# Performance work log

Measured on AMD Instinct MI355X. Metric: run time of the kernel, lower is better.

## Reference

```python
import jax, jax.numpy as jnp
import numpy as np

B = 256; SEED = 120; PRED = 24; D = 126; H = 1024
J = 14; JD = 9; HEADS = 4; DH = H // HEADS; SPLH = 128
PARENTS = (-1, -1, 0, 1, 2, 3, -1, 6, -1, -1, 8, 9, 10, 11)  # sparse SPL kinematic tree


def setup_inputs() -> dict:
    key = jax.random.key(0)
    ks = jax.random.split(key, 18)
    s = 0.02
    w = lambda k, shape: jax.random.normal(k, shape, dtype=jnp.float32) * s
    return {
        "poses": jax.random.normal(ks[0], (B, SEED + PRED, D), dtype=jnp.float32),
        "gru_Wih": w(ks[1], (3 * H, D)), "gru_Whh": w(ks[2], (3 * H, H)),
        "gru_bih": w(ks[3], (3 * H,)), "gru_bhh": w(ks[4], (3 * H,)),
        "pre_W": w(ks[5], (H, H)), "pre_b": w(ks[6], (H,)),
        "fp_W": w(ks[7], (H, D)), "fp_b": w(ks[8], (H,)),
        "inproj_W": w(ks[9], (3 * H, H)), "inproj_b": w(ks[10], (3 * H,)),
        "outproj_W": w(ks[11], (H, H)), "outproj_b": w(ks[12], (H,)),
        # per-joint SPL MLPs, stacked; root joints see zero-padded parent slot
        "spl_W1": w(ks[13], (J, SPLH, H + JD)), "spl_b1": w(ks[14], (J, SPLH)),
        "spl_W2": w(ks[15], (J, JD, SPLH)), "spl_b2": w(ks[16], (J, JD)),
    }


def _gru_cell(x, h, Wih, Whh, bih, bhh):
    gi = x @ Wih.T + bih
    gh = h @ Whh.T + bhh
    ir, iz, inn = jnp.split(gi, 3, axis=-1)
    hr, hz, hn = jnp.split(gh, 3, axis=-1)
    r = jax.nn.sigmoid(ir + hr)
    z = jax.nn.sigmoid(iz + hz)
    n = jnp.tanh(inn + r * hn)
    return (1.0 - z) * n + z * h


def _forward(poses, gru_Wih, gru_Whh, gru_bih, gru_bhh, pre_W, pre_b,
             fp_W, fp_b, inproj_W, inproj_b, outproj_W, outproj_b,
             spl_W1, spl_b1, spl_W2, spl_b2):
    input_seq = poses[:, :SEED]  # (B, T_in, D)
    # --- DCT motion attention (rFFT proxy) ---
    freq = jnp.fft.rfft(input_seq, axis=1).real          # (B, F, D), F = SEED//2+1
    feat = freq @ fp_W.T + fp_b                          # (B, F, H)
    qkv = feat @ inproj_W.T + inproj_b
    q, k, v = jnp.split(qkv, 3, axis=-1)
    hsplit = lambda t: t.reshape(t.shape[0], t.shape[1], HEADS, DH)
    q, k, v = hsplit(q), hsplit(k), hsplit(v)
    att = jax.nn.softmax(jnp.einsum('bqhd,bkhd->bhqk', q, k) / np.sqrt(DH).astype(np.float32), axis=-1)
    ctx = jnp.einsum('bhqk,bkhd->bqhd', att, v).reshape(feat.shape)
    attn_out = ctx @ outproj_W.T + outproj_b
    motion_ctx = attn_out.mean(axis=1)                   # (B, H)
    # --- GRU encode over seed ---
    h0 = jnp.zeros((poses.shape[0], H), dtype=poses.dtype)
    def enc(h, x):
        return _gru_cell(x, h, gru_Wih, gru_Whh, gru_bih, gru_bhh), None
    h, _ = jax.lax.scan(enc, h0, jnp.swapaxes(input_seq, 0, 1))
    x_last = input_seq[:, -1]
    # --- hierarchical SPL (sparse mode) ---
    def spl(hid):
        zero = jnp.zeros((hid.shape[0], JD), dtype=hid.dtype)
        preds = [None] * J
        for j in range(J):
            p = PARENTS[j]
            par = zero if p == -1 else preds[p]
            inp = jnp.concatenate([hid, par], axis=-1)   # (B, H+JD)
            hh = jax.nn.relu(inp @ spl_W1[j].T + spl_b1[j])
            preds[j] = jnp.tanh(hh @ spl_W2[j].T + spl_b2[j])
        return jnp.concatenate(preds, axis=-1)            # (B, J*JD)
    def dec(carry, _):
        x, hc = carry
        hc = _gru_cell(x, hc, gru_Wih, gru_Whh, gru_bih, gru_bhh)
        hid = jax.nn.relu(hc @ pre_W.T + pre_b) + motion_ctx
        x = x + spl(hid)
        return (x, hc), x
    _, ys = jax.lax.scan(dec, (x_last, h), None, length=PRED)
    return jnp.swapaxes(ys, 0, 1)                         # (B, PRED, D)


def reference(poses, gru_Wih, gru_Whh, gru_bih, gru_bhh, pre_W, pre_b,
              fp_W, fp_b, inproj_W, inproj_b, outproj_W, outproj_b,
              spl_W1, spl_b1, spl_W2, spl_b2):
    return _forward(poses, gru_Wih, gru_Whh, gru_bih, gru_bhh, pre_W, pre_b,
                    fp_W, fp_b, inproj_W, inproj_b, outproj_W, outproj_b,
                    spl_W1, spl_b1, spl_W2, spl_b2)
```

## Files before the change

kernel.cpp:

```cpp
#include <hip/hip_runtime.h>
#include <hip/hip_bf16.h>

typedef __hip_bfloat16 bf16;
typedef __attribute__((ext_vector_type(8))) short v8bf;
typedef __attribute__((ext_vector_type(16))) float f32x16;
typedef __attribute__((ext_vector_type(4))) float f32x4;
typedef unsigned long long ull;

#define B_    256
#define SEED_ 120
#define PRED_ 24
#define D_    126
#define H_    1024
#define F_    61
#define HEADS_ 4
#define DH_   256

#define GLD16(lds, g) __builtin_amdgcn_global_load_lds( \
    (const __attribute__((address_space(1))) unsigned int*)(g), \
    (__attribute__((address_space(3))) unsigned int*)(lds), 16, 0, 0)
#define VMWAIT(n) asm volatile("s_waitcnt vmcnt(" #n ")" ::: "memory")
#define BARRIER() do { __builtin_amdgcn_s_barrier(); __builtin_amdgcn_sched_barrier(0); } while(0)
#define AL(P) __hip_atomic_load((P), __ATOMIC_RELAXED, __HIP_MEMORY_SCOPE_AGENT)

// ... 45 lines not shown
  float v = (c < D_) ? poses[((size_t)b*(SEED_+PRED_) + (SEED_-1))*D_ + c] : 0.f;
  if (c < D_) x[b*D_ + c] = v;
  xpk[((b>>5)*4 + (c>>5))*1024 + (b&31)*32 + (c&31)] = __float2bfloat16(v);
}

__global__ void c_bf(const float* __restrict__ s, bf16* __restrict__ d, int n){
  int i = blockIdx.x*256 + threadIdx.x;
  if (i < n) d[i] = __float2bfloat16(s[i]);
}

__global__ void c_fpwt(const float* __restrict__ fpW, bf16* __restrict__ o){
  int dd = blockIdx.x;
  for (int k = threadIdx.x; k < H_; k += 256)
    o[(size_t)dd*H_ + k] = __float2bfloat16(dd < D_ ? fpW[(size_t)k*D_ + dd] : 0.f);
}

__global__ void c_wcat(const float* __restrict__ Wih, const float* __restrict__ Whh, bf16* __restrict__ o){
  int r = blockIdx.x;
  int jr; bool hasx, hash;
  if (r < 2048){ jr = r; hasx = true; hash = true; }
  else if (r < 3072){ jr = r; hasx = true; hash = false; }
  else { jr = r - 1024; hasx = false; hash = true; }
  bf16* row = o + (size_t)r*1152;
  for (int c = threadIdx.x; c < 1152; c += 256){
    float v = 0.f;
    if (c < D_) { if (hasx) v = Wih[(size_t)jr*D_ + c]; }
    else if (c >= 128){ if (hash) v = Whh[(size_t)jr*H_ + (c-128)]; }
    row[c] = __float2bfloat16(v);
  }
}

__global__ void c_bcat(const float* __restrict__ bih, const float* __restrict__ bhh, float* __restrict__ o){
  int r = blockIdx.x*256 + threadIdx.x;
  if (r >= 4096) return;
  float v;
  if (r < 2048) v = bih[r] + bhh[r];
  else if (r < 3072) v = bih[r];
  else v = bhh[r - 1024];
  o[r] = v;
}

__global__ __launch_bounds__(256) void c_wpk(const bf16* __restrict__ Wcat, bf16* __restrict__ Wpk){
  int chunk = blockIdx.x*4 + (threadIdx.x >> 6);
  int l = threadIdx.x & 63;
  int ks = chunk % 36; int t2 = chunk / 36; int g = t2 % 3; int ub = t2 / 3;
  int unit = ub*16 + (l & 15);
  bf16* dst = Wpk + (size_t)chunk*512 + l*8;
  #pragma unroll
  for (int e = 0; e < 8; ++e){
    int k = ks*32 + (l>>4)*8 + e;
    int row = (g==0) ? unit : (g==1) ? (1024+unit) : (k < 128 ? 2048+unit : 3072+unit);
    dst[e] = Wcat[(size_t)row*1152 + k];
  }
}

__global__ __launch_bounds__(256) void c_w1pk(const float* __restrict__ sW1, bf16* __restrict__ w1pk){
  int chunk = blockIdx.x*4 + (threadIdx.x >> 6);
  int l = threadIdx.x & 63;
  int ks = chunk & 31, ng = chunk >> 5;
  int unit = ng*16 + (l & 15);
  int j = unit >> 7, rr = unit & 127;
  bf16* dst = w1pk + (size_t)chunk*512 + l*8;
  #pragma unroll
  for (int e = 0; e < 8; ++e){
    int k = ks*32 + (l>>4)*8 + e;
    dst[e] = __float2bfloat16(sW1[((size_t)j*128 + rr)*1033 + k]);
  }
}

__global__ void c_w1par(const float* __restrict__ sW1, float* __restrict__ w1par){
  int i = blockIdx.x*256 + threadIdx.x;
  if (i < 14*9*128){
    int j = i / (9*128); int rem = i % (9*128); int ii = rem / 128; int th = rem % 128;
    w1par[i] = sW1[((size_t)(j*128 + th))*1033 + 1024 + ii];
  }
}

__global__ __launch_bounds__(256) void k_bc(const float* __restrict__ inW, const float* __restrict__ inb,
                     const float* __restrict__ fpb, float* __restrict__ bc){
  int wave = threadIdx.x >> 6, lane = threadIdx.x & 63;
  int r = blockIdx.x*4 + wave;
  const float4* row = (const float4*)(inW + (size_t)r*H_);
  const float4* fp4 = (const float4*)fpb;
  float s = 0.f;
  #pragma unroll
  for (int i = 0; i < 4; ++i){
    float4 a = row[lane + i*64];
    float4 b = fp4[lane + i*64];
    s += a.x*b.x + a.y*b.y + a.z*b.z + a.w*b.w;
  }
  #pragma unroll
  for (int off = 32; off; off >>= 1) s += __shfl_down(s, off);
  if (lane == 0) bc[r] = s + inb[r];
}

#define SLCP(QA, QB, KS, GACC) { \
  union { ull u[2]; v8bf v; } cc_; cc_.u[0]=(QA); cc_.u[1]=(QB); \
  v8bf a_ = cc_.v; \
  v8bf w0_ = *(const v8bf*)&Wl[(0*36+(KS))*512 + lane*8]; \
  v8bf w1_ = *(const v8bf*)&Wl[(1*36+(KS))*512 + lane*8]; \
  v8bf w2_ = *(const v8bf*)&Wl[(2*36+(KS))*512 + lane*8]; \
  aR = __builtin_amdgcn_mfma_f32_16x16x32_bf16(a_, w0_, aR, 0,0,0); \
  aZ = __builtin_amdgcn_mfma_f32_16x16x32_bf16(a_, w1_, aZ, 0,0,0); \
  GACC = __builtin_amdgcn_mfma_f32_16x16x32_bf16(a_, w2_, GACC, 0,0,0); }

#define LDHA(DA, DB, C) { \
// ... 96 lines not shown
    SLCP(a1,b1,25,aN) LDXP(a1,b1,t+1,1)
    SLCP(a2,b2,26,aN) LDXP(a2,b2,t+1,2)
    SLCP(a3,b3,27,aN) LDXP(a3,b3,t+1,3)
    SLCP(a4,b4,28,aN)
    SLCP(a5,b5,29,aN)
    SLCP(a6,b6,30,aN)
    SLCP(a7,b7,31,aN)
    SLCP(a8,b8,32,aN)
    SLCP(a9,b9,33,aN)
    SLCP(a10,b10,34,aN)
    SLCP(a11,b11,35,aN)

    bf16* hd = (t & 1) ? hpk0 : hpk1;
    const bool last = (t == nsteps-1);
    #pragma unroll
    for (int r = 0; r < 4; ++r){
      float rg = 1.f/(1.f + __expf(-(aR[r] + bR)));
      float zg = 1.f/(1.f + __expf(-(aZ[r] + bZ)));
      float ng = tanhf((aI[r] + bI) + rg*(aN[r] + bN));
      float hv = (1.f - zg)*ng + zg*hr[r];
      hr[r] = hv;
      bf16 hv16 = __float2bfloat16(hv);
      unsigned short hbits = *(unsigned short*)&hv16;
      __hip_atomic_store((unsigned short*)(hd + pwb + (size_t)(lb*4 + r)*32), hbits,
                         __ATOMIC_RELAXED, __HIP_MEMORY_SCOPE_AGENT);
      if (last){
        hout_plain[(size_t)(r0 + lb*4 + r)*1024 + ucol] = hv;
        if (hbplain) hbplain[(size_t)(r0 + lb*4 + r)*1024 + ucol] = __float2bfloat16(hv);
      }
    }
    if (coop && t + 1 < nsteps){
      VMWAIT(0);
      __syncthreads();
      if (tid == 0)
        __hip_atomic_store(&prog[q*64 + ub], (unsigned)(t+1), __ATOMIC_RELAXED, __HIP_MEMORY_SCOPE_AGENT);
    }
  }
}

__constant__ int LVJ[14] = {0,1,6,8,9, 2,3,7,10,11, 4,5,12,13};
__constant__ int LVO[4]  = {0,5,10,14};
__constant__ int PAR_[14] = {-1,-1,0,1,2,3,-1,6,-1,-1,8,9,10,11};

#define DGRL(S,C) { const ull* p_=(const ull*)(hspk + hbase + (size_t)(C)*1024); qa##S=AL(p_); qb##S=AL(p_+1); }
#define DGXL(S,C) { const ull* p_=(const ull*)(xpk + xbase + (size_t)(C)*1024); qa##S=AL(p_); qb##S=AL(p_+1); }
#define DGRC(S,KS,GACC) { union{ull u[2];v8bf v;}c_; c_.u[0]=qa##S;c_.u[1]=qb##S; v8bf a_=c_.v; \
  v8bf w0_=*(const v8bf*)&Wl[(KS)*512+lane*8]; \
  v8bf w1_=*(const v8bf*)&Wl[18432+(KS)*512+lane*8]; \
  v8bf w2_=*(const v8bf*)&Wl[36864+(KS)*512+lane*8]; \
  aR=__builtin_amdgcn_mfma_f32_16x16x32_bf16(a_,w0_,aR,0,0,0); \
  aZ=__builtin_amdgcn_mfma_f32_16x16x32_bf16(a_,w1_,aZ,0,0,0); \
  GACC=__builtin_amdgcn_mfma_f32_16x16x32_bf16(a_,w2_,GACC,0,0,0); }

__global__ __launch_bounds__(256) void gru_spl(
    const bf16* __restrict__ xpk, const bf16* __restrict__ Wpk,
    const float* __restrict__ bcat,
    const float* __restrict__ hin_plain, float* __restrict__ hout_plain,
    bf16* __restrict__ hbplain,
    const bf16* __restrict__ hspk, bf16* __restrict__ hdpk,
    const float* __restrict__ hhpre, const float* __restrict__ w1par,
    const float* __restrict__ sW2, const float* __restrict__ sb2,
    float* __restrict__ xcur, bf16* __restrict__ xpkw, float* __restrict__ out,
    int dt, unsigned* __restrict__ progS)
{
  __shared__ bf16 Wl[3*36*512];
  __shared__ float hhl[1792];
  __shared__ float preds_s[128];
  __shared__ float hh_s[128];
  const int tid = threadIdx.x, wave = tid >> 6, lane = tid & 63;
  const int bid = blockIdx.x;
  const int ub = bid & 63, q = bid >> 6, u0 = ub*16;

  {
    const bf16* wsrc = Wpk + (size_t)ub*(3*36*512);
    #pragma unroll
    for (int i = 0; i < 27; ++i){ int c = i*256 + tid; GLD16(&Wl[c*8], wsrc + (size_t)c*8); }
  }

  const int brow = bid, th = tid;
  if (dt > 0){
    for (int i = tid; i < 1792; i += 256) hhl[i] = hhpre[(size_t)brow*1792 + i];
    __syncthreads();
    for (int L = 0; L < 3; ++L){
      for (int ji = LVO[L]; ji < LVO[L+1]; ++ji){
        int j = LVJ[ji], p = PAR_[j];
        if (tid < 128){
          float a0s = hhl[j*128 + th];
          if (p >= 0){
            #pragma unroll
            for (int ii = 0; ii < 9; ++ii)
              a0s += w1par[(j*9 + ii)*128 + th] * preds_s[p*9 + ii];
          }
          hh_s[th] = fmaxf(a0s, 0.f);
        }
        __syncthreads();
        if (tid < 18){
          int oi = th >> 1, half = th & 1;
          const float4* w4 = (const float4*)(sW2 + (size_t)(j*9 + oi)*128 + half*64);
          float s = 0.f;
          #pragma unroll
          for (int q2 = 0; q2 < 16; ++q2){
            float4 wv = w4[q2];
            s += hh_s[half*64 + q2*4 + 0]*wv.x + hh_s[half*64 + q2*4 + 1]*wv.y
               + hh_s[half*64 + q2*4 + 2]*wv.z + hh_s[half*64 + q2*4 + 3]*wv.w;
          }
          s += __shfl_xor(s, 1);
          if (half == 0) preds_s[j*9 + oi] = tanhf(s + sb2[j*9 + oi]);
        }
        __syncthreads();
      }
    }
    if (tid < D_){
      int d = tid;
      size_t xi = (size_t)brow*D_ + d;
      float v = xcur[xi] + preds_s[d];
      xcur[xi] = v;
      bf16 v16 = __float2bfloat16(v);
      __hip_atomic_store((unsigned short*)(xpkw + ((size_t)(brow>>5)*4 + (d>>5))*1024 + (brow&31)*32 + (d&31)),
                         *(unsigned short*)&v16, __ATOMIC_RELAXED, __HIP_MEMORY_SCOPE_AGENT);
      out[((size_t)brow*PRED_ + (dt-1))*D_ + d] = v;
    }
    VMWAIT(0);
    __syncthreads();
    if (tid == 0)
      __hip_atomic_store(&progS[bid], (unsigned)dt, __ATOMIC_RELAXED, __HIP_MEMORY_SCOPE_AGENT);
  }

  VMWAIT(0); BARRIER();

  const int la = lane & 15, lb = lane >> 4;
  const int r0 = q*64 + wave*16;
  const int rb = r0 >> 5, y = wave & 1;
  const int ucol = u0 + la;
  const float bR = bcat[ucol], bZ = bcat[1024+ucol], bI = bcat[2048+ucol], bN = bcat[3072+ucol];
  const size_t hbase = (size_t)rb*32768 + (size_t)y*512 + la*32 + lb*8;
  const size_t xbase = (size_t)rb*4096  + (size_t)y*512 + la*32 + lb*8;
  const size_t pwb = (size_t)rb*32768 + (size_t)(u0>>5)*1024 + (size_t)y*512 + (u0&16) + la;

  float hr[4];
  #pragma unroll
  for (int r = 0; r < 4; ++r) hr[r] = hin_plain[(size_t)(r0 + lb*4 + r)*1024 + ucol];

  ull qa0,qa1,qa2,qa3,qa4,qa5,qa6,qa7,qa8,qa9,qa10,qa11;
  ull qb0,qb1,qb2,qb3,qb4,qb5,qb6,qb7,qb8,qb9,qb10,qb11;

  DGRL(0,0) DGRL(1,1) DGRL(2,2) DGRL(3,3) DGRL(4,4) DGRL(5,5)
  DGRL(6,6) DGRL(7,7) DGRL(8,8) DGRL(9,9) DGRL(10,10) DGRL(11,11)
  f32x4 z4 = {0.f,0.f,0.f,0.f};
  f32x4 aR = z4, aZ = z4, aI = z4, aN = z4;
  DGRC(0,4,aN)  DGRL(0,12)
  DGRC(1,5,aN)  DGRL(1,13)
  DGRC(2,6,aN)  DGRL(2,14)
  DGRC(3,7,aN)  DGRL(3,15)
  DGRC(4,8,aN)  DGRL(4,16)
  DGRC(5,9,aN)  DGRL(5,17)
  DGRC(6,10,aN) DGRL(6,18)
  DGRC(7,11,aN) DGRL(7,19)
  DGRC(8,12,aN) DGRL(8,20)
  DGRC(9,13,aN) DGRL(9,21)
  DGRC(10,14,aN) DGRL(10,22)
  DGRC(11,15,aN) DGRL(11,23)
  DGRC(0,16,aN) DGRL(0,24)
  DGRC(1,17,aN) DGRL(1,25)
  DGRC(2,18,aN) DGRL(2,26)
  DGRC(3,19,aN) DGRL(3,27)
  DGRC(4,20,aN) DGRL(4,28)
  DGRC(5,21,aN) DGRL(5,29)
  DGRC(6,22,aN) DGRL(6,30)
  DGRC(7,23,aN) DGRL(7,31)
  DGRC(8,24,aN)
  DGRC(9,25,aN)
  DGRC(10,26,aN)
  DGRC(11,27,aN)
  DGRC(0,28,aN)
  DGRC(1,29,aN)
  DGRC(2,30,aN)
  DGRC(3,31,aN)
  DGRC(4,32,aN)
  DGRC(5,33,aN)
  DGRC(6,34,aN)
  DGRC(7,35,aN)
  if (dt > 0){
    unsigned v = AL(&progS[wave*64 + lane]);
    while (__ballot(v >= (unsigned)dt) != ~0ULL){
      __builtin_amdgcn_s_sleep(2);
      v = AL(&progS[wave*64 + lane]);
    }
    __syncthreads();
    __builtin_amdgcn_sched_barrier(0);
  }
  DGXL(8,0) DGXL(9,1) DGXL(10,2) DGXL(11,3)
  DGRC(8,0,aI)
  DGRC(9,1,aI)
  DGRC(10,2,aI)
  DGRC(11,3,aI)
  #pragma unroll
  for (int r = 0; r < 4; ++r){
    float rg = 1.f/(1.f + __expf(-(aR[r] + bR)));
    float zg = 1.f/(1.f + __expf(-(aZ[r] + bZ)));
    float ng = tanhf((aI[r] + bI) + rg*(aN[r] + bN));
    float hv = (1.f - zg)*ng + zg*hr[r];
    bf16 hv16 = __float2bfloat16(hv);
    __hip_atomic_store((unsigned short*)(hdpk + pwb + (size_t)(lb*4 + r)*32),
                       *(unsigned short*)&hv16, __ATOMIC_RELAXED, __HIP_MEMORY_SCOPE_AGENT);
    hout_plain[(size_t)(r0 + lb*4 + r)*1024 + ucol] = hv;
    hbplain[(size_t)(r0 + lb*4 + r)*1024 + ucol] = hv16;
  }
}

#define W1L(S,C) { const ull* p_=(const ull*)(hidpk + w1abase + (size_t)(C)*1024); \
  qa##S=AL(p_); qb##S=AL(p_+1); \
  bq##S = *(const uint4*)(w1b0 + (size_t)(C)*512 + lane*8); \
  br##S = *(const uint4*)(w1b1 + (size_t)(C)*512 + lane*8); }
#define W1C(S) { union{ull u[2];v8bf v;}x_; x_.u[0]=qa##S;x_.u[1]=qb##S; \
  union{uint4 q; v8bf v;}b0_,b1_; b0_.q=bq##S; b1_.q=br##S; \
  c0=__builtin_amdgcn_mfma_f32_16x16x32_bf16(x_.v,b0_.v,c0,0,0,0); \
  c1=__builtin_amdgcn_mfma_f32_16x16x32_bf16(x_.v,b1_.v,c1,0,0,0); }

__global__ __launch_bounds__(512) void gemm_pw(
    const bf16* __restrict__ hb, const bf16* __restrict__ prebf,
    const float* __restrict__ preb, const float* __restrict__ motion,
    bf16* __restrict__ hidpk, const bf16* __restrict__ w1pk,
    const float* __restrict__ sb1, float* __restrict__ hhpre,
    int dt, unsigned* __restrict__ progP)
{
  __shared__ bf16 As[3][64*64];
  __shared__ bf16 Bs[3][64*64];
  const int tid = threadIdx.x, wave = tid >> 6, lane = tid & 63;
  const int bid = blockIdx.x;
  const int la = lane & 15, lb = lane >> 4;

  if (bid < 64){
    const int m0 = (bid & 3)*64, n0 = (bid >> 2)*64;
    const int fr = lane & 31, kh = lane >> 5;
    const int wm = (wave >> 1)*32, wn = (wave & 1)*32;
    f32x16 acc = {0.f,0.f,0.f,0.f,0.f,0.f,0.f,0.f,0.f,0.f,0.f,0.f,0.f,0.f,0.f,0.f};

    auto STAGE = [&](int buf, int kt){
      if (tid < 256){
        #pragma unroll
        for (int q2 = 0; q2 < 2; ++q2){
          int idx = q2*256 + tid;
          int row = idx >> 3, cp = idx & 7, csw = cp ^ (row & 7);
          GLD16(&As[buf][idx*8], hb + (size_t)(m0+row)*1024 + kt*64 + csw*8);
        }
        #pragma unroll
        for (int q2 = 0; q2 < 2; ++q2){
          int idx = q2*256 + tid;
          int row = idx >> 3, cp = idx & 7, csw = cp ^ (row & 7);
          GLD16(&Bs[buf][idx*8], prebf + (size_t)(n0+row)*1024 + kt*64 + csw*8);
        }
      }
    };
    auto COMPUTE = [&](int buf){
      if (wave < 4){
        const bf16* Ab = &As[buf][0];
        const bf16* Bb = &Bs[buf][0];
        #pragma unroll
        for (int ks = 0; ks < 4; ++ks){
          int ca = ks*2 + kh;
          v8bf av = *(const v8bf*)&Ab[(wm+fr)*64 + ((ca ^ ((wm+fr)&7))*8)];
          v8bf bv = *(const v8bf*)&Bb[(wn+fr)*64 + ((ca ^ ((wn+fr)&7))*8)];
          acc = __builtin_amdgcn_mfma_f32_32x32x16_bf16(av, bv, acc, 0, 0, 0);
        }
      }
    };

    STAGE(0, 0); STAGE(1, 1);
    VMWAIT(4); BARRIER();
    for (int kt = 0; kt < 16; ++kt){
      if (kt + 2 < 16) STAGE((kt+2)%3, kt+2);
      COMPUTE(kt%3);
      if (kt + 2 < 16){ VMWAIT(4); BARRIER(); }
      else if (kt + 1 < 16){ VMWAIT(0); BARRIER(); }
    }
    if (wave < 4){
      const int col = n0 + wn + fr;
      const float bb2 = preb[col];
      #pragma unroll
      for (int r = 0; r < 16; ++r){
        int row = m0 + wm + (r&3) + 8*(r>>2) + 4*kh;
        float v = fmaxf(acc[r] + bb2, 0.f) + motion[(size_t)row*1024 + col];
        bf16 v16 = __float2bfloat16(v);
        __hip_atomic_store((unsigned short*)(hidpk + ((size_t)(row>>5)*32 + (col>>5))*1024 + (row&31)*32 + (col&31)),
                           *(unsigned short*)&v16, __ATOMIC_RELAXED, __HIP_MEMORY_SCOPE_AGENT);
      }
    }
    VMWAIT(0);
    __syncthreads();
    if (tid == 0)
      __hip_atomic_store(&progP[bid], (unsigned)(dt+1), __ATOMIC_RELAXED, __HIP_MEMORY_SCOPE_AGENT);
  }

  if (wave == 0){
    unsigned v = AL(&progP[lane]);
    while (__ballot(v >= (unsigned)(dt+1)) != ~0ULL){
      __builtin_amdgcn_s_sleep(2);
      v = AL(&progP[lane]);
    }
  }
  __syncthreads();
  __builtin_amdgcn_sched_barrier(0);

  const int mq = bid / 28, ng = bid % 28;
  const int mg = wave >> 1, nc = wave & 1;
  const int r0w = mq*64 + mg*16;
  const int w1rb = r0w >> 5, w1y = mg & 1;
  const size_t w1abase = (size_t)w1rb*32768 + (size_t)w1y*512 + la*32 + lb*8;
  const int ug0 = ng*4 + nc*2, ug1 = ug0 + 1;
  const bf16* w1b0 = w1pk + (size_t)ug0*(32*512);
  const bf16* w1b1 = w1pk + (size_t)ug1*(32*512);
  const float sb1a = sb1[ug0*16 + la];
  const float sb1b = sb1[ug1*16 + la];

  ull qa0,qa1,qa2,qa3,qa4,qa5;
  ull qb0,qb1,qb2,qb3,qb4,qb5;
  uint4 bq0,bq1,bq2,bq3,bq4,bq5;
  uint4 br0,br1,br2,br3,br4,br5;

  W1L(0,0) W1L(1,1) W1L(2,2) W1L(3,3) W1L(4,4) W1L(5,5)
  f32x4 c0 = {0.f,0.f,0.f,0.f}, c1 = c0;
  W1C(0) W1L(0,6)
  W1C(1) W1L(1,7)
  W1C(2) W1L(2,8)
  W1C(3) W1L(3,9)
  W1C(4) W1L(4,10)
  W1C(5) W1L(5,11)
  W1C(0) W1L(0,12)
  W1C(1) W1L(1,13)
  W1C(2) W1L(2,14)
  W1C(3) W1L(3,15)
  W1C(4) W1L(4,16)
  W1C(5) W1L(5,17)
  W1C(0) W1L(0,18)
  W1C(1) W1L(1,19)
  W1C(2) W1L(2,20)
  W1C(3) W1L(3,21)
  W1C(4) W1L(4,22)
  W1C(5) W1L(5,23)
  W1C(0) W1L(0,24)
  W1C(1) W1L(1,25)
  W1C(2) W1L(2,26)
  W1C(3) W1L(3,27)
  W1C(4) W1L(4,28)
  W1C(5) W1L(5,29)
  W1C(0) W1L(0,30)
  W1C(1) W1L(1,31)
  W1C(2)
  W1C(3)
  W1C(4)
  W1C(5)
  W1C(0)
  W1C(1)
  #pragma unroll
  for (int r = 0; r < 4; ++r){
    int row = r0w + lb*4 + r;
    hhpre[(size_t)row*1792 + ug0*16 + la] = c0[r] + sb1a;
    hhpre[(size_t)row*1792 + ug1*16 + la] = c1[r] + sb1b;
  }
}

__global__ __launch_bounds__(256) void gemm64(
    const bf16* __restrict__ Am, const bf16* __restrict__ Bm, int K,
    const float* __restrict__ bias, const float* __restrict__ addmat,
    float* __restrict__ C, bf16* __restrict__ Cbf, int N, int MODE)
{
  __shared__ bf16 As[3][64*64];
  __shared__ bf16 Bs[3][64*64];
  const int tid = threadIdx.x;
  const int wave = tid >> 6, lane = tid & 63;
  const int m0 = blockIdx.x*64, n0 = blockIdx.y*64;
  const int fr = lane & 31, kh = lane >> 5;
  const int wm = (wave >> 1)*32, wn = (wave & 1)*32;
  const int KT = K >> 6;

  f32x16 acc = {0.f,0.f,0.f,0.f,0.f,0.f,0.f,0.f,0.f,0.f,0.f,0.f,0.f,0.f,0.f,0.f};

  auto STAGE = [&](int buf, int kt){
    #pragma unroll
    for (int q = 0; q < 2; ++q){
      int idx = q*256 + tid;
      int row = idx >> 3, cp = idx & 7, csw = cp ^ (row & 7);
      GLD16(&As[buf][idx*8], Am + (size_t)(m0+row)*K + kt*64 + csw*8);
    }
    #pragma unroll
    for (int q = 0; q < 2; ++q){
      int idx = q*256 + tid;
      int row = idx >> 3, cp = idx & 7, csw = cp ^ (row & 7);
      GLD16(&Bs[buf][idx*8], Bm + (size_t)(n0+row)*K + kt*64 + csw*8);
    }
  };
  auto COMPUTE = [&](int buf){
    const bf16* Ab = &As[buf][0];
    const bf16* Bb = &Bs[buf][0];
    #pragma unroll
    for (int ks = 0; ks < 4; ++ks){
      int ca = ks*2 + kh;
      v8bf av = *(const v8bf*)&Ab[(wm+fr)*64 + ((ca ^ ((wm+fr)&7))*8)];
      v8bf bv = *(const v8bf*)&Bb[(wn+fr)*64 + ((ca ^ ((wn+fr)&7))*8)];
      acc = __builtin_amdgcn_mfma_f32_32x32x16_bf16(av, bv, acc, 0, 0, 0);
    }
  };

  STAGE(0, 0);
  if (KT > 1){ STAGE(1, 1); VMWAIT(4); } else { VMWAIT(0); }
  BARRIER();
  for (int kt = 0; kt < KT; ++kt){
    if (kt + 2 < KT) STAGE((kt+2)%3, kt+2);
    COMPUTE(kt%3);
    if (kt + 2 < KT){ VMWAIT(4); BARRIER(); }
    else if (kt + 1 < KT){ VMWAIT(0); BARRIER(); }
// ... 112 lines not shown
      __syncthreads();
    }
  }
  for (int i = t; i < 4*D_; i += 128){
    int bb = i / D_, d = i % D_;
    int row = b0 + bb;
    size_t xi = (size_t)row*D_ + d;
    float v = x[xi] + preds_s[bb][d];
    x[xi] = v;
    xpk[((row>>5)*4 + (d>>5))*1024 + (row&31)*32 + (d&31)] = __float2bfloat16(v);
    out[((size_t)row*PRED_ + tstep)*D_ + d] = v;
  }
}

extern "C" void kernel_launch(void* const* d_in, const int* in_sizes, int n_in,
                              void* d_out, int out_size, void* d_ws, size_t ws_size,
                              hipStream_t stream){
  (void)in_sizes; (void)n_in; (void)out_size; (void)ws_size;
  const float* poses = (const float*)d_in[0];
  const float* gWih  = (const float*)d_in[1];
  const float* gWhh  = (const float*)d_in[2];
  const float* gbih  = (const float*)d_in[3];
  const float* gbhh  = (const float*)d_in[4];
  const float* preW  = (const float*)d_in[5];
  const float* preb  = (const float*)d_in[6];
  const float* fpW   = (const float*)d_in[7];
  const float* fpb   = (const float*)d_in[8];
  const float* inW   = (const float*)d_in[9];
  const float* inb   = (const float*)d_in[10];
  const float* outW  = (const float*)d_in[11];
  const float* outb  = (const float*)d_in[12];
  const float* sW1   = (const float*)d_in[13];
  const float* sb1   = (const float*)d_in[14];
  const float* sW2   = (const float*)d_in[15];
  const float* sb2   = (const float*)d_in[16];
  float* out = (float*)d_out;

  char* w = (char*)d_ws;
  size_t off = 0;
  auto alloc = [&](size_t bytes)->char*{ char* p = w + off; off += (bytes + 255) & ~(size_t)255; return p; };
  float* cosT   = (float*)alloc(7320*4);
  float* bc     = (float*)alloc(3072*4);
  float* motion = (float*)alloc((size_t)256*1024*4);
  float* hA     = (float*)alloc((size_t)256*1024*4);
  float* hB     = (float*)alloc((size_t)256*1024*4);
  float* xcur   = (float*)alloc((size_t)256*126*4);
  float* hhpre  = (float*)alloc((size_t)256*1792*4);
  float* bcat   = (float*)alloc(4096*4);
  float* w1par  = (float*)alloc(14*9*128*4);
  unsigned* prog= (unsigned*)alloc(4096);
  bf16* posespk = (bf16*)alloc((size_t)121*32768*2);
  bf16* Wcat    = (bf16*)alloc((size_t)4096*1152*2);
  bf16* Wpk     = (bf16*)alloc((size_t)64*108*512*2);
  bf16* w1pk    = (bf16*)alloc((size_t)112*32*512*2);
  bf16* prebf   = (bf16*)alloc((size_t)1024*1024*2);
  bf16* outbf   = (bf16*)alloc((size_t)1024*1024*2);
  bf16* inbf    = (bf16*)alloc((size_t)3072*1024*2);
  bf16* fpwt    = (bf16*)alloc((size_t)128*1024*2);
  bf16* ctxbf   = (bf16*)alloc((size_t)256*1024*2);
  bf16* hpkA    = (bf16*)alloc((size_t)256*1024*2);
  bf16* hpkB    = (bf16*)alloc((size_t)256*1024*2);
  bf16* hbplain = (bf16*)alloc((size_t)256*1024*2);
  bf16* hidpk   = (bf16*)alloc((size_t)256*1024*2);
  bf16* xpk     = (bf16*)alloc((size_t)32768*2);
  bf16* Wcbf    = (bf16*)alloc((size_t)3072*128*2);
  bf16* freqbf  = (bf16*)alloc((size_t)B_*F_*128*2);
  bf16* qkvbf   = (bf16*)alloc((size_t)15680*3072*2);

  hipMemsetAsync(hpkA, 0, (size_t)256*1024*2, stream);
  hipMemsetAsync(prog, 0, 4096, stream);

  k_cos<<<29, 256, 0, stream>>>(cosT);
  k_dft2<<<B_, 256, 0, stream>>>(poses, cosT, freqbf);
  c_poses<<<dim3(SEED_, B_), 128, 0, stream>>>(poses, posespk);
  c_xinit<<<B_, 128, 0, stream>>>(poses, xcur, xpk);
  c_wcat<<<4096, 256, 0, stream>>>(gWih, gWhh, Wcat);
  c_bcat<<<16, 256, 0, stream>>>(gbih, gbhh, bcat);
  c_wpk<<<1728, 256, 0, stream>>>(Wcat, Wpk);
  c_w1pk<<<896, 256, 0, stream>>>(sW1, w1pk);
  c_w1par<<<63, 256, 0, stream>>>(sW1, w1par);
  c_bf<<<4096, 256, 0, stream>>>(preW, prebf, 1024*1024);
  c_bf<<<4096, 256, 0, stream>>>(outW, outbf, 1024*1024);
  c_bf<<<12288, 256, 0, stream>>>(inW, inbf, 3072*1024);
  c_fpwt<<<128, 256, 0, stream>>>(fpW, fpwt);
  k_bc<<<768, 256, 0, stream>>>(inW, inb, fpb, bc);

  gemm64<<<dim3(48, 2), 256, 0, stream>>>(inbf, fpwt, 1024, nullptr, nullptr, nullptr, Wcbf, 128, 0);
  gemm64<<<dim3(244, 48), 256, 0, stream>>>(freqbf, Wcbf, 128, bc, nullptr, nullptr, qkvbf, 3072, 0);
  k_attn<<<dim3(HEADS_, B_), 256, 0, stream>>>(qkvbf, ctxbf);
  gemm64<<<dim3(4, 16), 256, 0, stream>>>(ctxbf, outbf, 1024, outb, nullptr, motion, nullptr, 1024, 0);

  {
    const bf16* a0 = posespk; int a1 = 32768; int a2 = SEED_; int a3 = 1;
    const bf16* a4 = Wpk; const float* a5 = bcat;
    const float* a6 = hA; float* a7 = hA; bf16* a8 = nullptr;
    bf16* a9 = hpkA; bf16* a10 = hpkB; unsigned* a11 = prog;
    void* args[] = { &a0, &a1, &a2, &a3, &a4, &a5, &a6, &a7, &a8, &a9, &a10, &a11 };
    hipLaunchCooperativeKernel(reinterpret_cast<void*>(gru_wave), dim3(256), dim3(256),
                               args, 0, stream);
  }

  float* hc = hA;  float* hn = hB;
  bf16* hpc = hpkA; bf16* hpn = hpkB;
  unsigned* progS = prog + 256;
  unsigned* progP = prog + 512;

  for (int t = 0; t < PRED_; ++t){
    gru_spl<<<256, 256, 0, stream>>>(xpk, Wpk, bcat, hc, hn, hbplain, hpc, hpn,
                                     hhpre, w1par, sW2, sb2, xcur, xpk, out, t, progS);
    { float* tf = hc; hc = hn; hn = tf; bf16* tb = hpc; hpc = hpn; hpn = tb; }
    gemm_pw<<<112, 512, 0, stream>>>(hbplain, prebf, preb, motion, hidpk, w1pk, sb1, hhpre, t, progP);
  }
  spl_all<<<64, 128, 0, stream>>>(hhpre, w1par, sW2, sb2, xcur, xpk, out, PRED_-1);
}
```

Measured before the change: 2.610 ms.

## Fuse GRU step, pre-projection GEMM and SPL W1 GEMM into one per-step kernel

Merges the per-step GRU kernel and the separate pre_W/SPL-W1 GEMM kernel into a single dec_step kernel. Inside, the phases are chained with device-wide progress flags. Each block now also caches a packed 16-unit slice of pre_W in LDS and computes its pre-projection directly from the freshly written packed hidden state. This removes the plain bf16 hidden copy and one kernel launch per decode step. The costs are more LDS per block, extra spin-wait barriers that depend on all blocks being co-resident, and in-place reuse of the hhpre buffer across phases.

```diff
diff --git a/kernel.cpp b/kernel.cpp
--- a/kernel.cpp
+++ b/kernel.cpp
@@ -121,6 +121,17 @@
     int row = (g==0) ? unit : (g==1) ? (1024+unit) : (k < 128 ? 2048+unit : 3072+unit);
     dst[e] = Wcat[(size_t)row*1152 + k];
   }
+}
+
+__global__ __launch_bounds__(256) void c_ppk(const float* __restrict__ preW, bf16* __restrict__ prepk){
+  int chunk = blockIdx.x*4 + (threadIdx.x >> 6);
+  int l = threadIdx.x & 63;
+  int ks = chunk & 31, ub = chunk >> 5;
+  int unit = ub*16 + (l & 15);
+  bf16* dst = prepk + (size_t)chunk*512 + l*8;
+  #pragma unroll
+  for (int e = 0; e < 8; ++e)
+    dst[e] = __float2bfloat16(preW[(size_t)unit*1024 + ks*32 + (l>>4)*8 + e]);
 }
 
 __global__ __launch_bounds__(256) void c_w1pk(const float* __restrict__ sW1, bf16* __restrict__ w1pk){
@@ -323,18 +334,40 @@
   aZ=__builtin_amdgcn_mfma_f32_16x16x32_bf16(a_,w1_,aZ,0,0,0); \
   GACC=__builtin_amdgcn_mfma_f32_16x16x32_bf16(a_,w2_,GACC,0,0,0); }
 
-__global__ __launch_bounds__(256) void gru_spl(
+#define PRL(S,C) { const ull* p_=(const ull*)(hdpk + hbase + (size_t)(C)*1024); qa##S=AL(p_); qb##S=AL(p_+1); }
+#define PRC(S,KS) { union{ull u[2];v8bf v;}c_; c_.u[0]=qa##S;c_.u[1]=qb##S; \
+  aP=__builtin_amdgcn_mfma_f32_16x16x32_bf16(c_.v, *(const v8bf*)&Wp[(KS)*512+lane*8], aP,0,0,0); }
+
+#define WLD(S,C) { const ull* p_=(const ull*)(hidpk + w1abase + (size_t)(C)*1024); \
+  wa##S=AL(p_); wb##S=AL(p_+1); \
+  wq##S##0 = *(const uint4*)(w1b0 + (size_t)(C)*512 + lane*8); \
+  wq##S##1 = *(const uint4*)(w1b1 + (size_t)(C)*512 + lane*8); \
+  wq##S##2 = *(const uint4*)(w1b2 + (size_t)(C)*512 + lane*8); \
+  wq##S##3 = *(const uint4*)(w1b3 + (size_t)(C)*512 + lane*8); }
+#define WCC(S) { union{ull u[2];v8bf v;}x_; x_.u[0]=wa##S;x_.u[1]=wb##S; \
+  union{uint4 q; v8bf v;}b_; \
+  b_.q=wq##S##0; c0=__builtin_amdgcn_mfma_f32_16x16x32_bf16(x_.v,b_.v,c0,0,0,0); \
+  b_.q=wq##S##1; c1=__builtin_amdgcn_mfma_f32_16x16x32_bf16(x_.v,b_.v,c1,0,0,0); \
+  b_.q=wq##S##2; c2=__builtin_amdgcn_mfma_f32_16x16x32_bf16(x_.v,b_.v,c2,0,0,0); \
+  b_.q=wq##S##3; c3=__builtin_amdgcn_mfma_f32_16x16x32_bf16(x_.v,b_.v,c3,0,0,0); }
+
+__global__ __launch_bounds__(256) void dec_step(
     const bf16* __restrict__ xpk, const bf16* __restrict__ Wpk,
     const float* __restrict__ bcat,
     const float* __restrict__ hin_plain, float* __restrict__ hout_plain,
-    bf16* __restrict__ hbplain,
     const bf16* __restrict__ hspk, bf16* __restrict__ hdpk,
-    const float* __restrict__ hhpre, const float* __restrict__ w1par,
+    const float* __restrict__ hhpre_in, float* __restrict__ hhpre_out,
+    const float* __restrict__ w1par,
     const float* __restrict__ sW2, const float* __restrict__ sb2,
+    const bf16* __restrict__ prepk, const float* __restrict__ preb,
+    const float* __restrict__ motion, bf16* __restrict__ hidpk,
+    const bf16* __restrict__ w1pk, const float* __restrict__ sb1,
     float* __restrict__ xcur, bf16* __restrict__ xpkw, float* __restrict__ out,
-    int dt, unsigned* __restrict__ progS)
+    int dt, unsigned* __restrict__ progS, unsigned* __restrict__ progG,
+    unsigned* __restrict__ progH)
 {
   __shared__ bf16 Wl[3*36*512];
+  __shared__ bf16 Wp[32*512];
   __shared__ float hhl[1792];
   __shared__ float preds_s[128];
   __shared__ float hh_s[128];
@@ -346,11 +379,14 @@
     const bf16* wsrc = Wpk + (size_t)ub*(3*36*512);
     #pragma unroll
     for (int i = 0; i < 27; ++i){ int c = i*256 + tid; GLD16(&Wl[c*8], wsrc + (size_t)c*8); }
+    const bf16* psrc = prepk + (size_t)ub*(32*512);
+    #pragma unroll
+    for (int i = 0; i < 8; ++i){ int c = i*256 + tid; GLD16(&Wp[c*8], psrc + (size_t)c*8); }
   }
 
   const int brow = bid, th = tid;
   if (dt > 0){
-    for (int i = tid; i < 1792; i += 256) hhl[i] = hhpre[(size_t)brow*1792 + i];
+    for (int i = tid; i < 1792; i += 256) hhl[i] = hhpre_in[(size_t)brow*1792 + i];
     __syncthreads();
     for (int L = 0; L < 3; ++L){
       for (int ji = LVO[L]; ji < LVO[L+1]; ++ji){
@@ -415,219 +451,204 @@
   ull qa0,qa1,qa2,qa3,qa4,qa5,qa6,qa7,qa8,qa9,qa10,qa11;
   ull qb0,qb1,qb2,qb3,qb4,qb5,qb6,qb7,qb8,qb9,qb10,qb11;
 
-  DGRL(0,0) DGRL(1,1) DGRL(2,2) DGRL(3,3) DGRL(4,4) DGRL(5,5)
-  DGRL(6,6) DGRL(7,7) DGRL(8,8) DGRL(9,9) DGRL(10,10) DGRL(11,11)
-  f32x4 z4 = {0.f,0.f,0.f,0.f};
-  f32x4 aR = z4, aZ = z4, aI = z4, aN = z4;
-  DGRC(0,4,aN)  DGRL(0,12)
-  DGRC(1,5,aN)  DGRL(1,13)
-  DGRC(2,6,aN)  DGRL(2,14)
-  DGRC(3,7,aN)  DGRL(3,15)
-  DGRC(4,8,aN)  DGRL(4,16)
-  DGRC(5,9,aN)  DGRL(5,17)
-  DGRC(6,10,aN) DGRL(6,18)
-  DGRC(7,11,aN) DGRL(7,19)
-  DGRC(8,12,aN) DGRL(8,20)
-  DGRC(9,13,aN) DGRL(9,21)
-  DGRC(10,14,aN) DGRL(10,22)
-  DGRC(11,15,aN) DGRL(11,23)
-  DGRC(0,16,aN) DGRL(0,24)
-  DGRC(1,17,aN) DGRL(1,25)
-  DGRC(2,18,aN) DGRL(2,26)
-  DGRC(3,19,aN) DGRL(3,27)
-  DGRC(4,20,aN) DGRL(4,28)
-  DGRC(5,21,aN) DGRL(5,29)
-  DGRC(6,22,aN) DGRL(6,30)
-  DGRC(7,23,aN) DGRL(7,31)
-  DGRC(8,24,aN)
-  DGRC(9,25,aN)
-  DGRC(10,26,aN)
-  DGRC(11,27,aN)
-  DGRC(0,28,aN)
-  DGRC(1,29,aN)
-  DGRC(2,30,aN)
-  DGRC(3,31,aN)
-  DGRC(4,32,aN)
-  DGRC(5,33,aN)
-  DGRC(6,34,aN)
-  DGRC(7,35,aN)
-  if (dt > 0){
-    unsigned v = AL(&progS[wave*64 + lane]);
-    while (__ballot(v >= (unsigned)dt) != ~0ULL){
+  {
+    DGRL(0,0) DGRL(1,1) DGRL(2,2) DGRL(3,3) DGRL(4,4) DGRL(5,5)
+    DGRL(6,6) DGRL(7,7) DGRL(8,8) DGRL(9,9) DGRL(10,10) DGRL(11,11)
+    f32x4 z4 = {0.f,0.f,0.f,0.f};
+    f32x4 aR = z4, aZ = z4, aI = z4, aN = z4;
+    DGRC(0,4,aN)  DGRL(0,12)
+    DGRC(1,5,aN)  DGRL(1,13)
+    DGRC(2,6,aN)  DGRL(2,14)
+    DGRC(3,7,aN)  DGRL(3,15)
+    DGRC(4,8,aN)  DGRL(4,16)
+    DGRC(5,9,aN)  DGRL(5,17)
+    DGRC(6,10,aN) DGRL(6,18)
+    DGRC(7,11,aN) DGRL(7,19)
+    DGRC(8,12,aN) DGRL(8,20)
+    DGRC(9,13,aN) DGRL(9,21)
+    DGRC(10,14,aN) DGRL(10,22)
+    DGRC(11,15,aN) DGRL(11,23)
+    DGRC(0,16,aN) DGRL(0,24)
+    DGRC(1,17,aN) DGRL(1,25)
+    DGRC(2,18,aN) DGRL(2,26)
+    DGRC(3,19,aN) DGRL(3,27)
+    DGRC(4,20,aN) DGRL(4,28)
+    DGRC(5,21,aN) DGRL(5,29)
+    DGRC(6,22,aN) DGRL(6,30)
+    DGRC(7,23,aN) DGRL(7,31)
+    DGRC(8,24,aN)
+    DGRC(9,25,aN)
+    DGRC(10,26,aN)
+    DGRC(11,27,aN)
+    DGRC(0,28,aN)
+    DGRC(1,29,aN)
+    DGRC(2,30,aN)
+    DGRC(3,31,aN)
+    DGRC(4,32,aN)
+    DGRC(5,33,aN)
+    DGRC(6,34,aN)
+    DGRC(7,35,aN)
+    if (dt > 0){
+      unsigned v = AL(&progS[wave*64 + lane]);
+      while (__ballot(v >= (unsigned)dt) != ~0ULL){
+        __builtin_amdgcn_s_sleep(2);
+        v = AL(&progS[wave*64 + lane]);
+      }
+      __syncthreads();
+      __builtin_amdgcn_sched_barrier(0);
+    }
+    DGXL(8,0) DGXL(9,1) DGXL(10,2) DGXL(11,3)
+    DGRC(8,0,aI)
+    DGRC(9,1,aI)
+    DGRC(10,2,aI)
+    DGRC(11,3,aI)
+    #pragma unroll
+    for (int r = 0; r < 4; ++r){
+      float rg = 1.f/(1.f + __expf(-(aR[r] + bR)));
+      float zg = 1.f/(1.f + __expf(-(aZ[r] + bZ)));
+      float ng = tanhf((aI[r] + bI) + rg*(aN[r] + bN));
+      float hv = (1.f - zg)*ng + zg*hr[r];
+      bf16 hv16 = __float2bfloat16(hv);
+      __hip_atomic_store((unsigned short*)(hdpk + pwb + (size_t)(lb*4 + r)*32),
+                         *(unsigned short*)&hv16, __ATOMIC_RELAXED, __HIP_MEMORY_SCOPE_AGENT);
+      hout_plain[(size_t)(r0 + lb*4 + r)*1024 + ucol] = hv;
+    }
+  }
+  VMWAIT(0);
+  __syncthreads();
+  if (tid == 0)
+    __hip_atomic_store(&progG[bid], (unsigned)(dt+1), __ATOMIC_RELAXED, __HIP_MEMORY_SCOPE_AGENT);
+
+  if (wave == 0){
+    unsigned v = AL(&progG[q*64 + lane]);
+    while (__ballot(v >= (unsigned)(dt+1)) != ~0ULL){
       __builtin_amdgcn_s_sleep(2);
-      v = AL(&progS[wave*64 + lane]);
+      v = AL(&progG[q*64 + lane]);
+    }
+  }
+  __syncthreads();
+  __builtin_amdgcn_sched_barrier(0);
+  {
+    PRL(0,0) PRL(1,1) PRL(2,2) PRL(3,3) PRL(4,4) PRL(5,5)
+    PRL(6,6) PRL(7,7) PRL(8,8) PRL(9,9) PRL(10,10) PRL(11,11)
+    f32x4 aP = {0.f,0.f,0.f,0.f};
+    PRC(0,0)  PRL(0,12)
+    PRC(1,1)  PRL(1,13)
+    PRC(2,2)  PRL(2,14)
+    PRC(3,3)  PRL(3,15)
+    PRC(4,4)  PRL(4,16)
+    PRC(5,5)  PRL(5,17)
+    PRC(6,6)  PRL(6,18)
+    PRC(7,7)  PRL(7,19)
+    PRC(8,8)  PRL(8,20)
+    PRC(9,9)  PRL(9,21)
+    PRC(10,10) PRL(10,22)
+    PRC(11,11) PRL(11,23)
+    PRC(0,12) PRL(0,24)
+    PRC(1,13) PRL(1,25)
+    PRC(2,14) PRL(2,26)
+    PRC(3,15) PRL(3,27)
+    PRC(4,16) PRL(4,28)
+    PRC(5,17) PRL(5,29)
+    PRC(6,18) PRL(6,30)
+    PRC(7,19) PRL(7,31)
+    PRC(8,20)
+    PRC(9,21)
+    PRC(10,22)
+    PRC(11,23)
+    PRC(0,24)
+    PRC(1,25)
+    PRC(2,26)
+    PRC(3,27)
+    PRC(4,28)
+    PRC(5,29)
+    PRC(6,30)
+    PRC(7,31)
+    const float pB = preb[ucol];
+    #pragma unroll
+    for (int r = 0; r < 4; ++r){
+      int row = r0 + lb*4 + r;
+      float v = fmaxf(aP[r] + pB, 0.f) + motion[(size_t)row*1024 + ucol];
+      bf16 v16 = __float2bfloat16(v);
+      __hip_atomic_store((unsigned short*)(hidpk + pwb + (size_t)(lb*4 + r)*32),
+                         *(unsigned short*)&v16, __ATOMIC_RELAXED, __HIP_MEMORY_SCOPE_AGENT);
+    }
+  }
+  VMWAIT(0);
+  __syncthreads();
+  if (tid == 0)
+    __hip_atomic_store(&progH[bid], (unsigned)(dt+1), __ATOMIC_RELAXED, __HIP_MEMORY_SCOPE_AGENT);
+
+  if (bid < 112){
+    const int mq = bid / 28, ng = bid % 28;
+    if (wave == 0){
+      unsigned v = AL(&progH[mq*64 + lane]);
+      while (__ballot(v >= (unsigned)(dt+1)) != ~0ULL){
+        __builtin_amdgcn_s_sleep(2);
+        v = AL(&progH[mq*64 + lane]);
+      }
     }
     __syncthreads();
     __builtin_amdgcn_sched_barrier(0);
-  }
-  DGXL(8,0) DGXL(9,1) DGXL(10,2) DGXL(11,3)
-  DGRC(8,0,aI)
-  DGRC(9,1,aI)
-  DGRC(10,2,aI)
-  DGRC(11,3,aI)
-  #pragma unroll
-  for (int r = 0; r < 4; ++r){
-    float rg = 1.f/(1.f + __expf(-(aR[r] + bR)));
-    float zg = 1.f/(1.f + __expf(-(aZ[r] + bZ)));
-    float ng = tanhf((aI[r] + bI) + rg*(aN[r] + bN));
-    float hv = (1.f - zg)*ng + zg*hr[r];
-    bf16 hv16 = __float2bfloat16(hv);
-    __hip_atomic_store((unsigned short*)(hdpk + pwb + (size_t)(lb*4 + r)*32),
-                       *(unsigned short*)&hv16, __ATOMIC_RELAXED, __HIP_MEMORY_SCOPE_AGENT);
-    hout_plain[(size_t)(r0 + lb*4 + r)*1024 + ucol] = hv;
-    hbplain[(size_t)(r0 + lb*4 + r)*1024 + ucol] = hv16;
-  }
-}
-
-#define W1L(S,C) { const ull* p_=(const ull*)(hidpk + w1abase + (size_t)(C)*1024); \
-  qa##S=AL(p_); qb##S=AL(p_+1); \
-  bq##S = *(const uint4*)(w1b0 + (size_t)(C)*512 + lane*8); \
-  br##S = *(const uint4*)(w1b1 + (size_t)(C)*512 + lane*8); }
-#define W1C(S) { union{ull u[2];v8bf v;}x_; x_.u[0]=qa##S;x_.u[1]=qb##S; \
-  union{uint4 q; v8bf v;}b0_,b1_; b0_.q=bq##S; b1_.q=br##S; \
-  c0=__builtin_amdgcn_mfma_f32_16x16x32_bf16(x_.v,b0_.v,c0,0,0,0); \
-  c1=__builtin_amdgcn_mfma_f32_16x16x32_bf16(x_.v,b1_.v,c1,0,0,0); }
-
-__global__ __launch_bounds__(512) void gemm_pw(
-    const bf16* __restrict__ hb, const bf16* __restrict__ prebf,
-    const float* __restrict__ preb, const float* __restrict__ motion,
-    bf16* __restrict__ hidpk, const bf16* __restrict__ w1pk,
-    const float* __restrict__ sb1, float* __restrict__ hhpre,
-    int dt, unsigned* __restrict__ progP)
-{
-  __shared__ bf16 As[3][64*64];
-  __shared__ bf16 Bs[3][64*64];
-  const int tid = threadIdx.x, wave = tid >> 6, lane = tid & 63;
-  const int bid = blockIdx.x;
-  const int la = lane & 15, lb = lane >> 4;
-
-  if (bid < 64){
-    const int m0 = (bid & 3)*64, n0 = (bid >> 2)*64;
-    const int fr = lane & 31, kh = lane >> 5;
-    const int wm = (wave >> 1)*32, wn = (wave & 1)*32;
-    f32x16 acc = {0.f,0.f,0.f,0.f,0.f,0.f,0.f,0.f,0.f,0.f,0.f,0.f,0.f,0.f,0.f,0.f};
-
-    auto STAGE = [&](int buf, int kt){
-      if (tid < 256){
-        #pragma unroll
-        for (int q2 = 0; q2 < 2; ++q2){
-          int idx = q2*256 + tid;
-          int row = idx >> 3, cp = idx & 7, csw = cp ^ (row & 7);
-          GLD16(&As[buf][idx*8], hb + (size_t)(m0+row)*1024 + kt*64 + csw*8);
-        }
-        #pragma unroll
-        for (int q2 = 0; q2 < 2; ++q2){
-          int idx = q2*256 + tid;
-          int row = idx >> 3, cp = idx & 7, csw = cp ^ (row & 7);
-          GLD16(&Bs[buf][idx*8], prebf + (size_t)(n0+row)*1024 + kt*64 + csw*8);
-        }
-      }
-    };
-    auto COMPUTE = [&](int buf){
-      if (wave < 4){
-        const bf16* Ab = &As[buf][0];
-        const bf16* Bb = &Bs[buf][0];
-        #pragma unroll
-        for (int ks = 0; ks < 4; ++ks){
-          int ca = ks*2 + kh;
-          v8bf av = *(const v8bf*)&Ab[(wm+fr)*64 + ((ca ^ ((wm+fr)&7))*8)];
-          v8bf bv = *(const v8bf*)&Bb[(wn+fr)*64 + ((ca ^ ((wn+fr)&7))*8)];
-          acc = __builtin_amdgcn_mfma_f32_32x32x16_bf16(av, bv, acc, 0, 0, 0);
-        }
-      }
-    };
-
-    STAGE(0, 0); STAGE(1, 1);
-    VMWAIT(4); BARRIER();
-    for (int kt = 0; kt < 16; ++kt){
-      if (kt + 2 < 16) STAGE((kt+2)%3, kt+2);
-      COMPUTE(kt%3);
-      if (kt + 2 < 16){ VMWAIT(4); BARRIER(); }
-      else if (kt + 1 < 16){ VMWAIT(0); BARRIER(); }
-    }
-    if (wave < 4){
-      const int col = n0 + wn + fr;
-      const float bb2 = preb[col];
-      #pragma unroll
-      for (int r = 0; r < 16; ++r){
-        int row = m0 + wm + (r&3) + 8*(r>>2) + 4*kh;
-        float v = fmaxf(acc[r] + bb2, 0.f) + motion[(size_t)row*1024 + col];
-        bf16 v16 = __float2bfloat16(v);
-        __hip_atomic_store((unsigned short*)(hidpk + ((size_t)(row>>5)*32 + (col>>5))*1024 + (row&31)*32 + (col&31)),
-                           *(unsigned short*)&v16, __ATOMIC_RELAXED, __HIP_MEMORY_SCOPE_AGENT);
-      }
-    }
-    VMWAIT(0);
-    __syncthreads();
-    if (tid == 0)
-      __hip_atomic_store(&progP[bid], (unsigned)(dt+1), __ATOMIC_RELAXED, __HIP_MEMORY_SCOPE_AGENT);
-  }
-
-  if (wave == 0){
-    unsigned v = AL(&progP[lane]);
-    while (__ballot(v >= (unsigned)(dt+1)) != ~0ULL){
-      __builtin_amdgcn_s_sleep(2);
-      v = AL(&progP[lane]);
-    }
-  }
-  __syncthreads();
-  __builtin_amdgcn_sched_barrier(0);
-
-  const int mq = bid / 28, ng = bid % 28;
-  const int mg = wave >> 1, nc = wave & 1;
-  const int r0w = mq*64 + mg*16;
-  const int w1rb = r0w >> 5, w1y = mg & 1;
-  const size_t w1abase = (size_t)w1rb*32768 + (size_t)w1y*512 + la*32 + lb*8;
-  const int ug0 = ng*4 + nc*2, ug1 = ug0 + 1;
-  const bf16* w1b0 = w1pk + (size_t)ug0*(32*512);
-  const bf16* w1b1 = w1pk + (size_t)ug1*(32*512);
-  const float sb1a = sb1[ug0*16 + la];
-  const float sb1b = sb1[ug1*16 + la];
-
-  ull qa0,qa1,qa2,qa3,qa4,qa5;
-  ull qb0,qb1,qb2,qb3,qb4,qb5;
-  uint4 bq0,bq1,bq2,bq3,bq4,bq5;
-  uint4 br0,br1,br2,br3,br4,br5;
-
-  W1L(0,0) W1L(1,1) W1L(2,2) W1L(3,3) W1L(4,4) W1L(5,5)
-  f32x4 c0 = {0.f,0.f,0.f,0.f}, c1 = c0;
-  W1C(0) W1L(0,6)
-  W1C(1) W1L(1,7)
-  W1C(2) W1L(2,8)
-  W1C(3) W1L(3,9)
-  W1C(4) W1L(4,10)
-  W1C(5) W1L(5,11)
-  W1C(0) W1L(0,12)
-  W1C(1) W1L(1,13)
-  W1C(2) W1L(2,14)
-  W1C(3) W1L(3,15)
-  W1C(4) W1L(4,16)
-  W1C(5) W1L(5,17)
-  W1C(0) W1L(0,18)
-  W1C(1) W1L(1,19)
-  W1C(2) W1L(2,20)
-  W1C(3) W1L(3,21)
-  W1C(4) W1L(4,22)
-  W1C(5) W1L(5,23)
-  W1C(0) W1L(0,24)
-  W1C(1) W1L(1,25)
-  W1C(2) W1L(2,26)
-  W1C(3) W1L(3,27)
-  W1C(4) W1L(4,28)
-  W1C(5) W1L(5,29)
-  W1C(0) W1L(0,30)
-  W1C(1) W1L(1,31)
-  W1C(2)
-  W1C(3)
-  W1C(4)
-  W1C(5)
-  W1C(0)
-  W1C(1)
-  #pragma unroll
-  for (int r = 0; r < 4; ++r){
-    int row = r0w + lb*4 + r;
-    hhpre[(size_t)row*1792 + ug0*16 + la] = c0[r] + sb1a;
-    hhpre[(size_t)row*1792 + ug1*16 + la] = c1[r] + sb1b;
+
+    const int r0w = mq*64 + wave*16;
+    const int w1rb = r0w >> 5, w1y = wave & 1;
+    const size_t w1abase = (size_t)w1rb*32768 + (size_t)w1y*512 + la*32 + lb*8;
+    const bf16* w1b0 = w1pk + (size_t)(ng*4 + 0)*(32*512);
+    const bf16* w1b1 = w1pk + (size_t)(ng*4 + 1)*(32*512);
+    const bf16* w1b2 = w1pk + (size_t)(ng*4 + 2)*(32*512);
+    const bf16* w1b3 = w1pk + (size_t)(ng*4 + 3)*(32*512);
+    const float s0 = sb1[(ng*4+0)*16 + la];
+    const float s1 = sb1[(ng*4+1)*16 + la];
+    const float s2 = sb1[(ng*4+2)*16 + la];
+    const float s3 = sb1[(ng*4+3)*16 + la];
+
+    ull wa0,wa1,wa2,wa3, wb0,wb1,wb2,wb3;
+    uint4 wq00,wq01,wq02,wq03, wq10,wq11,wq12,wq13;
+    uint4 wq20,wq21,wq22,wq23, wq30,wq31,wq32,wq33;
+
+    WLD(0,0) WLD(1,1) WLD(2,2) WLD(3,3)
+    f32x4 c0 = {0.f,0.f,0.f,0.f}, c1 = c0, c2 = c0, c3 = c0;
+    WCC(0) WLD(0,4)
+    WCC(1) WLD(1,5)
+    WCC(2) WLD(2,6)
+    WCC(3) WLD(3,7)
+    WCC(0) WLD(0,8)
+    WCC(1) WLD(1,9)
+    WCC(2) WLD(2,10)
+    WCC(3) WLD(3,11)
+    WCC(0) WLD(0,12)
+    WCC(1) WLD(1,13)
+    WCC(2) WLD(2,14)
+    WCC(3) WLD(3,15)
+    WCC(0) WLD(0,16)
+    WCC(1) WLD(1,17)
+    WCC(2) WLD(2,18)
+    WCC(3) WLD(3,19)
+    WCC(0) WLD(0,20)
+    WCC(1) WLD(1,21)
+    WCC(2) WLD(2,22)
+    WCC(3) WLD(3,23)
+    WCC(0) WLD(0,24)
+    WCC(1) WLD(1,25)
+    WCC(2) WLD(2,26)
+    WCC(3) WLD(3,27)
+    WCC(0) WLD(0,28)
+    WCC(1) WLD(1,29)
+    WCC(2) WLD(2,30)
+    WCC(3) WLD(3,31)
+    WCC(0)
+    WCC(1)
+    WCC(2)
+    WCC(3)
+    #pragma unroll
+    for (int r = 0; r < 4; ++r){
+      int row = r0w + lb*4 + r;
+      hhpre_out[(size_t)row*1792 + (ng*4+0)*16 + la] = c0[r] + s0;
+      hhpre_out[(size_t)row*1792 + (ng*4+1)*16 + la] = c1[r] + s1;
+      hhpre_out[(size_t)row*1792 + (ng*4+2)*16 + la] = c2[r] + s2;
+      hhpre_out[(size_t)row*1792 + (ng*4+3)*16 + la] = c3[r] + s3;
+    }
   }
 }
 
@@ -846,15 +867,14 @@
   bf16* posespk = (bf16*)alloc((size_t)121*32768*2);
   bf16* Wcat    = (bf16*)alloc((size_t)4096*1152*2);
   bf16* Wpk     = (bf16*)alloc((size_t)64*108*512*2);
+  bf16* prepk   = (bf16*)alloc((size_t)64*32*512*2);
   bf16* w1pk    = (bf16*)alloc((size_t)112*32*512*2);
-  bf16* prebf   = (bf16*)alloc((size_t)1024*1024*2);
   bf16* outbf   = (bf16*)alloc((size_t)1024*1024*2);
   bf16* inbf    = (bf16*)alloc((size_t)3072*1024*2);
   bf16* fpwt    = (bf16*)alloc((size_t)128*1024*2);
   bf16* ctxbf   = (bf16*)alloc((size_t)256*1024*2);
   bf16* hpkA    = (bf16*)alloc((size_t)256*1024*2);
   bf16* hpkB    = (bf16*)alloc((size_t)256*1024*2);
-  bf16* hbplain = (bf16*)alloc((size_t)256*1024*2);
   bf16* hidpk   = (bf16*)alloc((size_t)256*1024*2);
   bf16* xpk     = (bf16*)alloc((size_t)32768*2);
   bf16* Wcbf    = (bf16*)alloc((size_t)3072*128*2);
@@ -871,9 +891,9 @@
   c_wcat<<<4096, 256, 0, stream>>>(gWih, gWhh, Wcat);
   c_bcat<<<16, 256, 0, stream>>>(gbih, gbhh, bcat);
   c_wpk<<<1728, 256, 0, stream>>>(Wcat, Wpk);
+  c_ppk<<<512, 256, 0, stream>>>(preW, prepk);
   c_w1pk<<<896, 256, 0, stream>>>(sW1, w1pk);
   c_w1par<<<63, 256, 0, stream>>>(sW1, w1par);
-  c_bf<<<4096, 256, 0, stream>>>(preW, prebf, 1024*1024);
   c_bf<<<4096, 256, 0, stream>>>(outW, outbf, 1024*1024);
   c_bf<<<12288, 256, 0, stream>>>(inW, inbf, 3072*1024);
   c_fpwt<<<128, 256, 0, stream>>>(fpW, fpwt);
@@ -897,13 +917,15 @@
   float* hc = hA;  float* hn = hB;
   bf16* hpc = hpkA; bf16* hpn = hpkB;
   unsigned* progS = prog + 256;
-  unsigned* progP = prog + 512;
+  unsigned* progG = prog + 512;
+  unsigned* progH = prog + 768;
 
   for (int t = 0; t < PRED_; ++t){
-    gru_spl<<<256, 256, 0, stream>>>(xpk, Wpk, bcat, hc, hn, hbplain, hpc, hpn,
-                                     hhpre, w1par, sW2, sb2, xcur, xpk, out, t, progS);
+    dec_step<<<256, 256, 0, stream>>>(xpk, Wpk, bcat, hc, hn, hpc, hpn,
+                                      hhpre, hhpre, w1par, sW2, sb2,
+                                      prepk, preb, motion, hidpk, w1pk, sb1,
+                                      xcur, xpk, out, t, progS, progG, progH);
     { float* tf = hc; hc = hn; hn = tf; bf16* tb = hpc; hpc = hpn; hpn = tb; }
-    gemm_pw<<<112, 512, 0, stream>>>(hbplain, prebf, preb, motion, hidpk, w1pk, sb1, hhpre, t, progP);
   }
   spl_all<<<64, 128, 0, stream>>>(hhpre, w1par, sW2, sb2, xcur, xpk, out, PRED_-1);
 }
```

Measured after the change: 2.358 ms. 9.7% less time.
